# Optimization experiments

Hardware: AMD Instinct MI355X
Metric: run time of the kernel (lower is better)

## Reference

```python
import jax, jax.numpy as jnp
import numpy as np

B, N, D = 32, 4096, 512
HID = 64
MIN_K, MAX_K = 3, 50
IN_DIM = 3 * D + 5  # mean/max/std pooled features + 5 structural features
NEG_SENTINEL = -1e8


def setup_inputs() -> dict:
    key = jax.random.key(0)
    ks = jax.random.split(key, 9)
    x = jax.random.normal(ks[0], (B, N, D), dtype=jnp.float32)
    keep = jax.random.uniform(ks[1], (B, 1, N)) < 0.75
    mask = jnp.where(keep, 0.0, -1e9).astype(jnp.float32)
    def lin(k, fan_in, fan_out):
        bound = 1.0 / np.sqrt(fan_in)
        kw, kb = jax.random.split(k)
        W = jax.random.uniform(kw, (fan_in, fan_out), minval=-bound, maxval=bound, dtype=jnp.float32)
        b = jax.random.uniform(kb, (fan_out,), minval=-bound, maxval=bound, dtype=jnp.float32)
        return W, b
    W1, b1 = lin(ks[2], IN_DIM, HID)
    W2, b2 = lin(ks[3], HID, HID // 2)
    W3, b3 = lin(ks[4], HID // 2, 1)
    return {"x": x, "mask": mask, "W1": W1, "b1": b1, "W2": W2, "b2": b2, "W3": W3, "b3": b3}


def reference(x, mask, W1, b1, W2, b2, W3, b3):
    valid = mask[:, 0, :] > NEG_SENTINEL            # [B, N] bool
    m = valid.astype(x.dtype)[..., None]            # [B, N, 1]
    cnt = m.sum(axis=1)                             # [B, 1] valid-node counts
    cnt_safe = jnp.maximum(cnt, 1.0)
    has_nodes = cnt > 0.0                           # [B, 1]

    # masked mean / max / unbiased std pooling (segment-reduce over nodes)
    x_mean = (x * m).sum(axis=1) / cnt_safe                                    # [B, D]
    x_mean = jnp.where(has_nodes, x_mean, 0.0)
    x_max = jnp.where(valid[..., None], x, -jnp.inf).max(axis=1)               # [B, D]
    x_max = jnp.where(has_nodes, x_max, 0.0)
    var = (m * (x - x_mean[:, None, :]) ** 2).sum(axis=1) / jnp.maximum(cnt - 1.0, 1.0)
    x_std = jnp.where(has_nodes, jnp.sqrt(var), 0.0)                           # [B, D]

    # structural features: dense path with no edge_index -> constants except log_size
    n = cnt[:, 0]
    log_size = jnp.log(n + 1.0) / 5.0
    ones = jnp.ones_like(log_size)
    # [log_size, density=0.1, avg_degree/10=0.2, max_degree=4.0, degree_std/10=0.1]
    sf = jnp.stack([log_size, 0.1 * ones, 0.2 * ones, 4.0 * ones, 0.1 * ones], axis=1)  # [B, 5]

    g = jnp.concatenate([x_mean, x_max, x_std, sf], axis=1)   # [B, 3D+5]
    h = jax.nn.relu(g @ W1 + b1)                              # dropout is identity in eval
    h = jax.nn.relu(h @ W2 + b2)
    score = jax.nn.sigmoid(h @ W3 + b3)[:, 0]                 # [B]

    num_clusters_cont = MIN_K + score * (MAX_K - MIN_K)
    num_clusters = jnp.round(num_clusters_cont).mean().astype(jnp.int32)
    num_clusters = jnp.clip(num_clusters, MIN_K, MAX_K)
    return num_clusters, score.mean()
```

## Files before the change

### kernel.cpp

```cpp
#include <hip/hip_runtime.h>
#include <cmath>

#define B_      32
#define N_      4096
#define D_      512
#define D4      (D_/4)
#define NCH     64
#define RPC     64
#define IN_DIM  1541
#define GSTRIDE 1568
#define NSPLIT  8
#define CHUNK   193
#define NEG_SENT (-1.0e8f)
#define BIGNEG   (1.0e30f)

__global__ __launch_bounds__(128) void stats_partial_kernel(
    const float* __restrict__ x, const float* __restrict__ mask,
    float4* __restrict__ psum, float4* __restrict__ psq,
    float4* __restrict__ pmax, float* __restrict__ pcnt)
{
    __shared__ float sw[RPC];
    __shared__ float so[RPC];
    const int tx = threadIdx.x;
    const int c  = blockIdx.x;
    const int b  = blockIdx.y;

    if (tx < RPC) {
        const float mv = mask[b * N_ + c * RPC + tx];
        const float w  = (mv > NEG_SENT) ? 1.f : 0.f;
        sw[tx] = w;
        so[tx] = (w - 1.f) * BIGNEG;
        float cv = w;
        #pragma unroll
        for (int off = 32; off > 0; off >>= 1) cv += __shfl_down(cv, off);
        if (tx == 0) pcnt[b * NCH + c] = cv;
    }
    __syncthreads();

    const float4* __restrict__ xb =
        (const float4*)x + ((size_t)b * N_ + (size_t)c * RPC) * D4 + tx;

    float4 s  = {0,0,0,0};
    float4 q  = {0,0,0,0};
    float4 mx = {-BIGNEG,-BIGNEG,-BIGNEG,-BIGNEG};

    #pragma unroll 4
    for (int j = 0; j < RPC; ++j) {
        const float4 v = xb[(size_t)j * D4];
        const float  w = sw[j];
        const float  o = so[j];
        const float tvx = v.x*w, tvy = v.y*w, tvz = v.z*w, tvw = v.w*w;
        s.x += tvx; s.y += tvy; s.z += tvz; s.w += tvw;
        q.x = fmaf(tvx, v.x, q.x); q.y = fmaf(tvy, v.y, q.y);
        q.z = fmaf(tvz, v.z, q.z); q.w = fmaf(tvw, v.w, q.w);
        mx.x = fmaxf(mx.x, fmaf(w, v.x, o));
        mx.y = fmaxf(mx.y, fmaf(w, v.y, o));
        mx.z = fmaxf(mx.z, fmaf(w, v.z, o));
        mx.w = fmaxf(mx.w, fmaf(w, v.w, o));
    }

    const size_t idx = ((size_t)(b * NCH + c)) * D4 + tx;
    psum[idx] = s; psq[idx] = q; pmax[idx] = mx;
}

__global__ __launch_bounds__(256) void combine_g_kernel(
    const float4* __restrict__ psum, const float4* __restrict__ psq,
    const float4* __restrict__ pmax, const float* __restrict__ pcnt,
    float* __restrict__ g_all)
{
    __shared__ float4 Ss[2][D4], Sq[2][D4], Sm[2][D4];
    __shared__ float scnt;

    const int tid = threadIdx.x;
    const int tx  = tid & 127;
    const int ty  = tid >> 7;
    const int b   = blockIdx.x;

    {
        float4 s = {0,0,0,0}, q = {0,0,0,0};
        float4 mx = {-BIGNEG,-BIGNEG,-BIGNEG,-BIGNEG};
        const int c0 = ty * (NCH/2);
        #pragma unroll 4
        for (int c = c0; c < c0 + NCH/2; ++c) {
            const size_t idx = ((size_t)(b * NCH + c)) * D4 + tx;
            float4 a = psum[idx], u = psq[idx], w = pmax[idx];
            s.x += a.x; s.y += a.y; s.z += a.z; s.w += a.w;
            q.x += u.x; q.y += u.y; q.z += u.z; q.w += u.w;
            mx.x = fmaxf(mx.x,w.x); mx.y = fmaxf(mx.y,w.y);
            mx.z = fmaxf(mx.z,w.z); mx.w = fmaxf(mx.w,w.w);
        }
        Ss[ty][tx] = s; Sq[ty][tx] = q; Sm[ty][tx] = mx;
    }
    if (tid < 64) {
        float cv = pcnt[b * NCH + tid];
        #pragma unroll
        for (int off = 32; off > 0; off >>= 1) cv += __shfl_down(cv, off);
        if (tid == 0) scnt = cv;
    }
    __syncthreads();

    const float cnt = scnt;
    float* __restrict__ g = g_all + (size_t)b * GSTRIDE;
    if (ty == 0) {
        float4 s = Ss[0][tx], s_ = Ss[1][tx];
        float4 q = Sq[0][tx], q_ = Sq[1][tx];
        float4 mx = Sm[0][tx], m_ = Sm[1][tx];
        s.x += s_.x; s.y += s_.y; s.z += s_.z; s.w += s_.w;
        q.x += q_.x; q.y += q_.y; q.z += q_.z; q.w += q_.w;
        mx.x = fmaxf(mx.x,m_.x); mx.y = fmaxf(mx.y,m_.y);
        mx.z = fmaxf(mx.z,m_.z); mx.w = fmaxf(mx.w,m_.w);

        const bool  has = cnt > 0.f;
        const float inv = 1.f / fmaxf(cnt, 1.f);
        const float dn  = 1.f / fmaxf(cnt - 1.f, 1.f);
        float sa[4] = {s.x,s.y,s.z,s.w};
        float qa[4] = {q.x,q.y,q.z,q.w};
        float ma[4] = {mx.x,mx.y,mx.z,mx.w};
        #pragma unroll
        for (int k = 0; k < 4; ++k) {
            const int d = 4*tx + k;
            const float mn = has ? sa[k] * inv : 0.f;
            const float vv = fmaxf((qa[k] - cnt * mn * mn) * dn, 0.f);
            g[d]        = mn;
            g[D_ + d]   = has ? ma[k] : 0.f;
            g[2*D_ + d] = has ? sqrtf(vv) : 0.f;
        }
        if (tx == 0) {
            g[3*D_ + 0] = logf(cnt + 1.f) * 0.2f;
            g[3*D_ + 1] = 0.1f;
            g[3*D_ + 2] = 0.2f;
            g[3*D_ + 3] = 4.0f;
            g[3*D_ + 4] = 0.1f;
        }
    }
}

__global__ __launch_bounds__(64) void layer1_kernel(
    const float* __restrict__ g_all, const float* __restrict__ W1,
    float* __restrict__ h1p)
{
    __shared__ float sg[CHUNK];
    const int o  = threadIdx.x;
    const int c  = blockIdx.x;
    const int b  = blockIdx.y;
    const int i0 = c * CHUNK;
    const int len = (IN_DIM - i0) < CHUNK ? (IN_DIM - i0) : CHUNK;

    for (int j = o; j < len; j += 64) sg[j] = g_all[(size_t)b * GSTRIDE + i0 + j];
    __syncthreads();

    const float* __restrict__ Wp = W1 + (size_t)i0 * 64 + o;
    float a = 0.f;
    #pragma unroll 8
    for (int k = 0; k < len; ++k)
        a = fmaf(sg[k], Wp[(size_t)k * 64], a);
    h1p[((size_t)b * NSPLIT + c) * 64 + o] = a;
}

__global__ __launch_bounds__(1024) void finish_kernel(
    const float* __restrict__ h1p, const float* __restrict__ b1,
    const float* __restrict__ W2, const float* __restrict__ b2,
    const float* __restrict__ W3, const float* __restrict__ b3,
    float* __restrict__ out)
{
    __shared__ float h1s[B_ * 64];
    __shared__ float h2s[B_ * 33];
    const int tid = threadIdx.x;

    #pragma unroll
    for (int r = 0; r < 2; ++r) {
        const int oi = tid + r * 1024;
        const int b = oi >> 6, o = oi & 63;
        float a = b1[o];
        #pragma unroll
        for (int c = 0; c < NSPLIT; ++c) a += h1p[((size_t)b * NSPLIT + c) * 64 + o];
        h1s[oi] = fmaxf(a, 0.f);
    }
    __syncthreads();

    {
        const int b = tid >> 5, o = tid & 31;
        float a = b2[o];
        #pragma unroll
        for (int i = 0; i < 64; ++i) a = fmaf(h1s[b*64 + i], W2[i*32 + o], a);
        h2s[b*33 + o] = fmaxf(a, 0.f);
    }
    __syncthreads();

    if (tid < 32) {
        const int b = tid;
        float a = b3[0];
        #pragma unroll
        for (int i = 0; i < 32; ++i) a = fmaf(h2s[b*33 + i], W3[i], a);
        float sc = 1.f / (1.f + expf(-a));
        float r  = rintf(3.f + sc * 47.f);
        #pragma unroll
        for (int off = 16; off > 0; off >>= 1) {
            sc += __shfl_down(sc, off);
            r  += __shfl_down(r,  off);
        }
        if (tid == 0) {
            const float mean_r = r * (1.f / 32.f);
            int nc = (int)mean_r;
            nc = nc < 3 ? 3 : (nc > 50 ? 50 : nc);
            out[0] = (float)nc;
            out[1] = sc * (1.f / 32.f);
        }
    }
}

extern "C" void kernel_launch(void* const* d_in, const int* in_sizes, int n_in,
                              void* d_out, int out_size, void* d_ws, size_t ws_size,
                              hipStream_t stream)
{
    const float* x    = (const float*)d_in[0];
    const float* mask = (const float*)d_in[1];
    const float* W1   = (const float*)d_in[2];
    const float* b1   = (const float*)d_in[3];
    const float* W2   = (const float*)d_in[4];
    const float* b2   = (const float*)d_in[5];
    const float* W3   = (const float*)d_in[6];
    const float* b3   = (const float*)d_in[7];
    float* out = (float*)d_out;

    const size_t PCOUNT = (size_t)B_ * NCH * D4;
    float4* psum = (float4*)d_ws;
    float4* psq  = psum + PCOUNT;
    float4* pmax = psq  + PCOUNT;
    float*  pcnt = (float*)(pmax + PCOUNT);
    float*  g_all = pcnt + (size_t)B_ * NCH;
    float*  h1p   = g_all + (size_t)B_ * GSTRIDE;

    dim3 gridA(NCH, B_);
    stats_partial_kernel<<<gridA, 128, 0, stream>>>(x, mask, psum, psq, pmax, pcnt);
    combine_g_kernel<<<B_, 256, 0, stream>>>(psum, psq, pmax, pcnt, g_all);
    dim3 gridL1(NSPLIT, B_);
    layer1_kernel<<<gridL1, 64, 0, stream>>>(g_all, W1, h1p);
    finish_kernel<<<1, 1024, 0, stream>>>(h1p, b1, W2, b2, W3, b3, out);
}
```

Measured before the change: 397.1 us.

## Compact valid rows via ballot and skip loading padded nodes in stats pass

The stats kernel now builds a compacted list of valid row indices per chunk using wave ballots and prefix popcounts, then loops only over valid rows. Padded rows are never loaded, which removes about a quarter of the HBM reads of x, and the mask multiply and offset arithmetic go away. Chunks are enlarged to 128 rows (32 chunks per batch), halving the partial buffers read by the combine kernel. The cost is a data-dependent loop trip count and gathered row accesses, which are still coalesced within each row.

```diff
diff --git a/kernel.cpp b/kernel.cpp
--- a/kernel.cpp
+++ b/kernel.cpp
@@ -5,8 +5,8 @@
 #define N_      4096
 #define D_      512
 #define D4      (D_/4)
-#define NCH     64
-#define RPC     64
+#define NCH     32
+#define RPC     128
 #define IN_DIM  1541
 #define GSTRIDE 1568
 #define NSPLIT  8
@@ -19,23 +19,27 @@
     float4* __restrict__ psum, float4* __restrict__ psq,
     float4* __restrict__ pmax, float* __restrict__ pcnt)
 {
-    __shared__ float sw[RPC];
-    __shared__ float so[RPC];
-    const int tx = threadIdx.x;
-    const int c  = blockIdx.x;
-    const int b  = blockIdx.y;
-
-    if (tx < RPC) {
+    __shared__ int sidx[RPC];
+    __shared__ int swc0, swc1;
+    const int tx   = threadIdx.x;
+    const int wave = tx >> 6;
+    const int lane = tx & 63;
+    const int c    = blockIdx.x;
+    const int b    = blockIdx.y;
+
+    {
         const float mv = mask[b * N_ + c * RPC + tx];
-        const float w  = (mv > NEG_SENT) ? 1.f : 0.f;
-        sw[tx] = w;
-        so[tx] = (w - 1.f) * BIGNEG;
-        float cv = w;
-        #pragma unroll
-        for (int off = 32; off > 0; off >>= 1) cv += __shfl_down(cv, off);
-        if (tx == 0) pcnt[b * NCH + c] = cv;
-    }
-    __syncthreads();
+        const bool pred = mv > NEG_SENT;
+        const unsigned long long bal = __ballot(pred);
+        const int prefix = __popcll(bal & ((1ull << lane) - 1ull));
+        if (lane == 0) { if (wave == 0) swc0 = __popcll(bal); else swc1 = __popcll(bal); }
+        __syncthreads();
+        const int base = (wave == 0) ? 0 : swc0;
+        if (pred) sidx[base + prefix] = tx;
+    }
+    __syncthreads();
+    const int m = swc0 + swc1;
+    if (tx == 0) pcnt[b * NCH + c] = (float)m;
 
     const float4* __restrict__ xb =
         (const float4*)x + ((size_t)b * N_ + (size_t)c * RPC) * D4 + tx;
@@ -45,18 +49,14 @@
     float4 mx = {-BIGNEG,-BIGNEG,-BIGNEG,-BIGNEG};
 
     #pragma unroll 4
-    for (int j = 0; j < RPC; ++j) {
-        const float4 v = xb[(size_t)j * D4];
-        const float  w = sw[j];
-        const float  o = so[j];
-        const float tvx = v.x*w, tvy = v.y*w, tvz = v.z*w, tvw = v.w*w;
-        s.x += tvx; s.y += tvy; s.z += tvz; s.w += tvw;
-        q.x = fmaf(tvx, v.x, q.x); q.y = fmaf(tvy, v.y, q.y);
-        q.z = fmaf(tvz, v.z, q.z); q.w = fmaf(tvw, v.w, q.w);
-        mx.x = fmaxf(mx.x, fmaf(w, v.x, o));
-        mx.y = fmaxf(mx.y, fmaf(w, v.y, o));
-        mx.z = fmaxf(mx.z, fmaf(w, v.z, o));
-        mx.w = fmaxf(mx.w, fmaf(w, v.w, o));
+    for (int i = 0; i < m; ++i) {
+        const int r = sidx[i];
+        const float4 v = xb[(size_t)r * D4];
+        s.x += v.x; s.y += v.y; s.z += v.z; s.w += v.w;
+        q.x = fmaf(v.x, v.x, q.x); q.y = fmaf(v.y, v.y, q.y);
+        q.z = fmaf(v.z, v.z, q.z); q.w = fmaf(v.w, v.w, q.w);
+        mx.x = fmaxf(mx.x, v.x); mx.y = fmaxf(mx.y, v.y);
+        mx.z = fmaxf(mx.z, v.z); mx.w = fmaxf(mx.w, v.w);
     }
 
     const size_t idx = ((size_t)(b * NCH + c)) * D4 + tx;
@@ -91,10 +91,10 @@
         }
         Ss[ty][tx] = s; Sq[ty][tx] = q; Sm[ty][tx] = mx;
     }
-    if (tid < 64) {
+    if (tid < NCH) {
         float cv = pcnt[b * NCH + tid];
         #pragma unroll
-        for (int off = 32; off > 0; off >>= 1) cv += __shfl_down(cv, off);
+        for (int off = 16; off > 0; off >>= 1) cv += __shfl_down(cv, off);
         if (tid == 0) scnt = cv;
     }
     __syncthreads();
```

Measured after the change: 380.9 us. 1.04x faster.
